# Performance work log

Measured on AMD Instinct MI355X. Metric: run time of the kernel, lower is better.

The kernel has to match this reference:

```python
import jax, jax.numpy as jnp
import numpy as np
import math

D_MODEL = 1024
LAYER_ID = 6
NUM_LAYERS = 12
B = 8
T = 2048


def setup_inputs() -> dict:
    key = jax.random.key(0)
    ks = jax.random.split(key, 5)
    r01 = LAYER_ID / (NUM_LAYERS - 1)
    r1a0 = 1.0 - LAYER_ID / NUM_LAYERS
    h = np.arange(D_MODEL, dtype=np.float32)
    w = (-5.0 + 8.0 * (h / (D_MODEL - 1)) ** (0.7 + 1.3 * r01)).astype(np.float32)
    zigzag = np.array([(i + 1) % 3 - 1 for i in range(D_MODEL)], np.float32) * 0.5
    u = (np.ones(D_MODEL, np.float32) * math.log(0.3) + zigzag).astype(np.float32)
    xinit = (h / D_MODEL).astype(np.float32)
    tmk = (xinit ** r1a0).reshape(1, 1, D_MODEL).astype(np.float32)
    tmv = (tmk + 0.3 * r01).astype(np.float32)
    tmr = (xinit ** (0.5 * r1a0)).reshape(1, 1, D_MODEL).astype(np.float32)
    s = 1.0 / math.sqrt(D_MODEL)
    Wk = jax.random.normal(ks[0], (D_MODEL, D_MODEL), jnp.float32) * s
    Wv = jax.random.normal(ks[1], (D_MODEL, D_MODEL), jnp.float32) * s
    Wr = jax.random.normal(ks[2], (D_MODEL, D_MODEL), jnp.float32) * s
    Wo = jax.random.normal(ks[3], (D_MODEL, D_MODEL), jnp.float32) * s
    x = jax.random.normal(ks[4], (B, T, D_MODEL), jnp.float32)
    return dict(
        x=x,
        w=jnp.asarray(w), u=jnp.asarray(u),
        time_mix_k=jnp.asarray(tmk), time_mix_v=jnpp if False else jnp.asarray(tmv), time_mix_r=jnp.asarray(tmr),
        Wk=Wk, Wv=Wv, Wr=Wr, Wo=Wo,
    )


def _wkv(w, u, k, v):
    # w,u: [C] (raw params); k,v: [B,T,C]. Numerically-stable RWKV scan.
    wn = -jnp.exp(w)  # decay (negative)

    def step(carry, kv):
        aa, bb, pp = carry  # each [B,C]
        kt, vt = kv         # [B,C]
        ww = u + kt
        p = jnp.maximum(pp, ww)
        e1 = jnp.exp(pp - p)
        e2 = jnp.exp(ww - p)
        y = (e1 * aa + e2 * vt) / (e1 * bb + e2)
        ww2 = pp + wn
        p2 = jnp.maximum(ww2, kt)
        e1b = jnp.exp(ww2 - p2)
        e2b = jnp.exp(kt - p2)
        return (e1b * aa + e2b * vt, e1b * bb + e2b, p2), y

    Bd, Td, Cd = k.shape
    init = (jnp.zeros((Bd, Cd), k.dtype), jnp.zeros((Bd, Cd), k.dtype),
            jnp.full((Bd, Cd), -1e38, k.dtype))
    kT = jnp.swapaxes(k, 0, 1)  # [T,B,C]
    vT = jnp.swapaxes(v, 0, 1)
    _, ys = jax.lax.scan(step, init, (kT, vT))
    return jnp.swapaxes(ys, 0, 1)  # [B,T,C]


def reference(x, w, u, time_mix_k, time_mix_v, time_mix_r, Wk, Wv, Wr, Wo):
    # token shift: zero-pad one step at the front of time, drop last
    xs = jnp.pad(x, ((0, 0), (1, 0), (0, 0)))[:, :-1]
    xk = x * time_mix_k + xs * (1.0 - time_mix_k)
    xv = x * time_mix_v + xs * (1.0 - time_mix_v)
    xr = x * time_mix_r + xs * (1.0 - time_mix_r)
    k = jnp.einsum('btc,dc->btd', xk, Wk)
    v = jnp.einsum('btc,dc->btd', xv, Wv)
    r = jnp.einsum('btc,dc->btd', xr, Wr)
    wkv = _wkv(w, u, k, v)
    rwkv = jax.nn.sigmoid(r) * wkv
    return jnp.einsum('btc,dc->btd', rwkv, Wo)
```

## Files before the change

kernel.cpp:

```cpp
#include <hip/hip_runtime.h>
#include <hip/hip_bf16.h>
#include <stdint.h>

#define DM     1024
#define BATCH  8
#define SEQ    2048
#define MROWS  (BATCH * SEQ)
#define NCH    16
#define CHL    (SEQ / NCH)

typedef unsigned short u16;
typedef __attribute__((ext_vector_type(8))) __bf16 bf16x8;
typedef __attribute__((ext_vector_type(4))) float  f32x4;

#define MB (1024ull * 1024ull)

__device__ __forceinline__ u16 f2bf(float f) {
    unsigned u = __float_as_uint(f);
    u += 0x7fffu + ((u >> 16) & 1u);
    return (u16)(u >> 16);
}
__device__ __forceinline__ float bf2f(u16 h) {
    return __uint_as_float(((unsigned)h) << 16);
}

__device__ __forceinline__ bool in_f32(const void* wraw) {
    return ((*(const unsigned*)wraw) & 0xFFFFu) == 0u;
}

__device__ __forceinline__ void ld16_lds(const u16* g, u16* l) {
    __builtin_amdgcn_global_load_lds(
        (const __attribute__((address_space(1))) void*)g,
        (__attribute__((address_space(3))) void*)l, 16, 0, 0);
}

__global__ __launch_bounds__(256) void mix_tile(
    const void* __restrict__ xraw,
    const void* __restrict__ tmkraw,
    const void* __restrict__ tmvraw,
    const void* __restrict__ tmrraw,
    const void* __restrict__ wraw,
    u16* __restrict__ xk, u16* __restrict__ xv, u16* __restrict__ xr)
{
    __shared__ u16 xt[18 * 1024];
    const bool f32i = in_f32(wraw);
    const int r0  = blockIdx.x * 16;
    const int t0  = r0 & (SEQ - 1);
    const int tid = threadIdx.x;
    const int c4  = tid * 4;

    float mk[4], mv[4], mr[4];
    if (f32i) {
        #pragma unroll
        for (int j = 0; j < 4; ++j) {
            mk[j] = ((const float*)tmkraw)[c4 + j];
            mv[j] = ((const float*)tmvraw)[c4 + j];
            mr[j] = ((const float*)tmrraw)[c4 + j];
        }
    } else {
        union { u16 h[4]; uint2 u; } a, b, c;
        a.u = *(const uint2*)((const u16*)tmkraw + c4);
        b.u = *(const uint2*)((const u16*)tmvraw + c4);
        c.u = *(const uint2*)((const u16*)tmrraw + c4);
        #pragma unroll
        for (int j = 0; j < 4; ++j) {
            mk[j] = bf2f(a.h[j]); mv[j] = bf2f(b.h[j]); mr[j] = bf2f(c.h[j]);
        }
    }

    #pragma unroll
    for (int p = 0; p < 9; ++p) {
        int lr = 2 * p + (tid >> 7);
        int gr = r0 - 1 + lr;
        if (lr == 0 && t0 == 0) gr = r0;
        if (gr >= MROWS) gr = r0;
        if (f32i) {
            const float* gp = (const float*)xraw + (size_t)gr * DM + (tid & 127) * 8;
            union { u16 h[8]; uint4 u; } t;
            #pragma unroll
            for (int j = 0; j < 8; ++j) t.h[j] = f2bf(gp[j]);
            *(uint4*)&xt[p * 2048 + tid * 8] = t.u;
        } else {
            const u16* gp = (const u16*)xraw + (size_t)gr * DM + (tid & 127) * 8;
            ld16_lds(gp, &xt[p * 2048 + (tid >> 6) * 512]);
        }
    }
    __syncthreads();

    const size_t obase = (size_t)r0 * DM + c4;
    #pragma unroll 4
    for (int rr = 0; rr < 16; ++rr) {
        union { u16 h[4]; uint2 u; } xa, xsv, ok, ov, orr;
        xa.u = *(const uint2*)&xt[(rr + 1) * 1024 + c4];
        float xf[4], sf[4];
        if (rr == 0 && t0 == 0) {
            #pragma unroll
            for (int j = 0; j < 4; ++j) sf[j] = 0.f;
        } else {
            xsv.u = *(const uint2*)&xt[rr * 1024 + c4];
            #pragma unroll
            for (int j = 0; j < 4; ++j) sf[j] = bf2f(xsv.h[j]);
        }
        #pragma unroll
        for (int j = 0; j < 4; ++j) xf[j] = bf2f(xa.h[j]);
        #pragma unroll
        for (int j = 0; j < 4; ++j) {
            float d = xf[j] - sf[j];
            ok.h[j]  = f2bf(sf[j] + mk[j] * d);
            ov.h[j]  = f2bf(sf[j] + mv[j] * d);
            orr.h[j] = f2bf(sf[j] + mr[j] * d);
        }
        size_t o = obase + (size_t)rr * DM;
        *(uint2*)(xk + o) = ok.u;
        *(uint2*)(xv + o) = ov.u;
        *(uint2*)(xr + o) = orr.u;
    }
}

__global__ void cast_w(const void* __restrict__ Wraw,
                       const void* __restrict__ wflag,
                       u16* __restrict__ Wb)
{
    int i = (blockIdx.x * 256 + threadIdx.x) << 2;
    if (in_f32(wflag)) {
        float4 wv = *(const float4*)((const float*)Wraw + i);
        union { u16 h[4]; uint2 u; } p;
        p.h[0] = f2bf(wv.x); p.h[1] = f2bf(wv.y);
        p.h[2] = f2bf(wv.z); p.h[3] = f2bf(wv.w);
        *(uint2*)(Wb + i) = p.u;
    } else {
        *(uint2*)(Wb + i) = *(const uint2*)((const u16*)Wraw + i);
    }
}

__device__ __forceinline__ void store_out(float* p, float v) { *p = v; }
__device__ __forceinline__ void store_out(u16*  p, float v) { *p = f2bf(v); }

template <typename OUT>
__global__ __launch_bounds__(256) void gemm_bt(const u16* __restrict__ A,
                                               const u16* __restrict__ B,
                                               OUT* __restrict__ C,
                                               int M, int N, int K)
{
    __shared__ u16 As[128 * 64];
    __shared__ u16 Bs[128 * 64];
    const int tid  = threadIdx.x;
    const int wave = tid >> 6, lane = tid & 63;
    const int wm   = wave >> 1, wn = wave & 1;
    const int lr   = lane & 15, quad = lane >> 4;
    const int tm   = blockIdx.y * 128, tn = blockIdx.x * 128;
    const int srow  = lane >> 3;
    const int skoff = (lane & 7) * 8;

    f32x4 acc[4][4] = {};

    for (int k0 = 0; k0 < K; k0 += 64) {
        #pragma unroll
        for (int i2 = 0; i2 < 4; ++i2) {
            int ch  = wave * 4 + i2;
            int row = ch * 8 + srow;
            ld16_lds(A + (size_t)(tm + row) * K + k0 + skoff, &As[ch * 512]);
            ld16_lds(B + (size_t)(tn + row) * K + k0 + skoff, &Bs[ch * 512]);
        }
        __syncthreads();
        #pragma unroll
        for (int kk2 = 0; kk2 < 2; ++kk2) {
            bf16x8 af[4], bfg[4];
            #pragma unroll
            for (int mi = 0; mi < 4; ++mi)
                af[mi] = *(const bf16x8*)&As[(wm * 64 + mi * 16 + lr) * 64 + kk2 * 32 + quad * 8];
            #pragma unroll
            for (int ni = 0; ni < 4; ++ni)
                bfg[ni] = *(const bf16x8*)&Bs[(wn * 64 + ni * 16 + lr) * 64 + kk2 * 32 + quad * 8];
            #pragma unroll
            for (int mi = 0; mi < 4; ++mi)
                #pragma unroll
                for (int ni = 0; ni < 4; ++ni)
                    acc[mi][ni] = __builtin_amdgcn_mfma_f32_16x16x32_bf16(
                        af[mi], bfg[ni], acc[mi][ni], 0, 0, 0);
        }
        __syncthreads();
    }
    #pragma unroll
    for (int mi = 0; mi < 4; ++mi)
        #pragma unroll
        for (int ni = 0; ni < 4; ++ni)
            #pragma unroll
            for (int r = 0; r < 4; ++r) {
                int row = tm + wm * 64 + mi * 16 + quad * 4 + r;
                int col = tn + wn * 64 + ni * 16 + lr;
                store_out(&C[(size_t)row * N + col], acc[mi][ni][r]);
            }
}

__device__ __forceinline__ float ldval(const float* p) { return *p; }
__device__ __forceinline__ float ldval(const u16*  p) { return bf2f(*p); }

template <typename KT>
__global__ __launch_bounds__(256) void wkv_phase1(
    const KT* __restrict__ kk, const u16* __restrict__ vv,
    const void* __restrict__ wraw,
    float* __restrict__ sa, float* __restrict__ sb, float* __restrict__ sp)
{
    const int gid = blockIdx.x * 256 + threadIdx.x;
    const int c   = gid & (DM - 1);
    const int ch  = (gid >> 10) & (NCH - 1);
    const int b   = gid >> 14;
    float wc = in_f32(wraw) ? ((const float*)wraw)[c] : bf2f(((const u16*)wraw)[c]);
    const float wn = -__expf(wc);

    const size_t base = ((size_t)b * SEQ + (size_t)ch * CHL) * DM + c;
    float la = 0.f, lb = 0.f, lp = -1e38f;

    float kb[8], vb[8];
    #pragma unroll
    for (int j = 0; j < 8; ++j) {
        size_t id = base + (size_t)j * DM;
        kb[j] = ldval(kk + id); vb[j] = ldval(vv + id);
    }
    for (int t0 = 0; t0 < CHL; t0 += 8) {
        const bool more = (t0 + 8) < CHL;
        float kn[8], vn[8];
        if (more) {
            size_t nb = base + (size_t)(t0 + 8) * DM;
            #pragma unroll
            for (int j = 0; j < 8; ++j) {
                size_t id = nb + (size_t)j * DM;
                kn[j] = ldval(kk + id); vn[j] = ldval(vv + id);
            }
        }
        #pragma unroll
        for (int j = 0; j < 8; ++j) {
            const float kt = kb[j], vt = vb[j];
            const float w2 = lp + wn;
            const float p2 = fmaxf(w2, kt);
            const float e1 = __expf(w2 - p2);
            const float e2 = __expf(kt - p2);
            la = e1 * la + e2 * vt;
            lb = e1 * lb + e2;
            lp = p2;
        }
        if (more) {
            #pragma unroll
            for (int j = 0; j < 8; ++j) { kb[j] = kn[j]; vb[j] = vn[j]; }
        }
    }
    const int sidx = ((b * NCH + ch) << 10) + c;
    sa[sidx] = la; sb[sidx] = lb; sp[sidx] = lp;
}

__global__ __launch_bounds__(256) void wkv_combine(
    float* __restrict__ sa, float* __restrict__ sb, float* __restrict__ sp,
    const void* __restrict__ wraw)
{
    const int gid = blockIdx.x * 256 + threadIdx.x;
    const int c   = gid & (DM - 1);
    const int b   = gid >> 10;
    float wc = in_f32(wraw) ? ((const float*)wraw)[c] : bf2f(((const u16*)wraw)[c]);
    const float lamL = -__expf(wc) * (float)CHL;

    float aa = 0.f, bb = 0.f, pp = -1e38f;
    #pragma unroll
    for (int j = 0; j < NCH; ++j) {
        const int idx = ((b * NCH + j) << 10) + c;
        const float la = sa[idx], lb = sb[idx], lp = sp[idx];
        sa[idx] = aa; sb[idx] = bb; sp[idx] = pp;
        const float w2 = pp + lamL;
        const float np = fmaxf(w2, lp);
        const float e1 = __expf(w2 - np);
        const float e2 = __expf(lp - np);
        aa = e1 * aa + e2 * la;
        bb = e1 * bb + e2 * lb;
        pp = np;
    }
}

template <typename KT>
__global__ __launch_bounds__(256) void wkv_phase3(
    const KT* __restrict__ kk, const u16* __restrict__ vv,
    const u16* __restrict__ rr,
    const float* __restrict__ sa, const float* __restrict__ sb,
    const float* __restrict__ sp,
    const void* __restrict__ wraw, const void* __restrict__ uraw,
    u16* __restrict__ out)
{
    const int gid = blockIdx.x * 256 + threadIdx.x;
    const int c   = gid & (DM - 1);
    const int ch  = (gid >> 10) & (NCH - 1);
    const int b   = gid >> 14;
    float wc, uc;
    if (in_f32(wraw)) {
        wc = ((const float*)wraw)[c]; uc = ((const float*)uraw)[c];
    } else {
        wc = bf2f(((const u16*)wraw)[c]); uc = bf2f(((const u16*)uraw)[c]);
    }
    const float wn = -__expf(wc);
    const float uu = uc;

    const int sidx = ((b * NCH + ch) << 10) + c;
    float aa = sa[sidx], bb = sb[sidx], pp = sp[sidx];

    const size_t base = ((size_t)b * SEQ + (size_t)ch * CHL) * DM + c;

    float kb[8], vb[8], rb[8];
    #pragma unroll
    for (int j = 0; j < 8; ++j) {
        size_t id = base + (size_t)j * DM;
        kb[j] = ldval(kk + id); vb[j] = ldval(vv + id); rb[j] = ldval(rr + id);
    }
    for (int t0 = 0; t0 < CHL; t0 += 8) {
        const bool more = (t0 + 8) < CHL;
        float kn[8], vn[8], rn[8];
        if (more) {
            size_t nb = base + (size_t)(t0 + 8) * DM;
            #pragma unroll
            for (int j = 0; j < 8; ++j) {
                size_t id = nb + (size_t)j * DM;
                kn[j] = ldval(kk + id); vn[j] = ldval(vv + id); rn[j] = ldval(rr + id);
            }
        }
        #pragma unroll
        for (int j = 0; j < 8; ++j) {
            const float kt = kb[j], vt = vb[j], rt = rb[j];
            const float ww = uu + kt;
            const float p  = fmaxf(pp, ww);
            const float e1 = __expf(pp - p);
            const float e2 = __expf(ww - p);
            const float y  = (e1 * aa + e2 * vt) / (e1 * bb + e2);
            const float w2 = pp + wn;
            const float p2 = fmaxf(w2, kt);
            const float e1b = __expf(w2 - p2);
            const float e2b = __expf(kt - p2);
            aa = e1b * aa + e2b * vt;
            bb = e1b * bb + e2b;
            pp = p2;
            const float sr = 1.f / (1.f + __expf(-rt));
            out[base + (size_t)(t0 + j) * DM] = f2bf(sr * y);
        }
        if (more) {
            #pragma unroll
            for (int j = 0; j < 8; ++j) { kb[j] = kn[j]; vb[j] = vn[j]; rb[j] = rn[j]; }
        }
    }
}

extern "C" void kernel_launch(void* const* d_in, const int* in_sizes, int n_in,
                              void* d_out, int out_size, void* d_ws, size_t ws_size,
                              hipStream_t stream)
{
    const void* x   = d_in[0];
    const void* w   = d_in[1];
    const void* u   = d_in[2];
    const void* tmk = d_in[3];
    const void* tmv = d_in[4];
    const void* tmr = d_in[5];
    const void* Wk  = d_in[6];
    const void* Wv  = d_in[7];
    const void* Wr  = d_in[8];
    const void* Wo  = d_in[9];

    char* base = (char*)d_ws;
    const bool kf32 = ws_size >= 168 * MB;
    u16* Wkb  = (u16*)(base);
    u16* Wvb  = (u16*)(base + 2 * MB);
    u16* Wrb  = (u16*)(base + 4 * MB);
    u16* Wob  = (u16*)(base + 6 * MB);
    u16* xk   = (u16*)(base + 8 * MB);
    u16* xv   = (u16*)(base + 40 * MB);
    u16* xr   = (u16*)(base + 72 * MB);
    void* kbuf = (void*)(base + 104 * MB);
    u16* vb   = xk;
    u16* rb   = xv;
    u16* rwkv = xr;
    float* sa = (float*)(base);
    float* sbuf = (float*)(base + 512 * 1024);
    float* sp = (float*)(base + 1024 * 1024);

    cast_w<<<DM * DM / 1024, 256, 0, stream>>>(Wk, w, Wkb);
    cast_w<<<DM * DM / 1024, 256, 0, stream>>>(Wv, w, Wvb);
    cast_w<<<DM * DM / 1024, 256, 0, stream>>>(Wr, w, Wrb);
    cast_w<<<DM * DM / 1024, 256, 0, stream>>>(Wo, w, Wob);
    mix_tile<<<MROWS / 16, 256, 0, stream>>>(x, tmk, tmv, tmr, w, xk, xv, xr);

    dim3 gg(DM / 128, MROWS / 128);
    if (kf32) {
        gemm_bt<float><<<gg, 256, 0, stream>>>(xk, Wkb, (float*)kbuf, MROWS, DM, DM);
    } else {
        gemm_bt<u16><<<gg, 256, 0, stream>>>(xk, Wkb, (u16*)kbuf, MROWS, DM, DM);
    }
    gemm_bt<u16><<<gg, 256, 0, stream>>>(xv, Wvb, vb, MROWS, DM, DM);
    gemm_bt<u16><<<gg, 256, 0, stream>>>(xr, Wrb, rb, MROWS, DM, DM);

    const int scan_threads = BATCH * NCH * DM;
    if (kf32) {
        wkv_phase1<float><<<scan_threads / 256, 256, 0, stream>>>(
            (const float*)kbuf, vb, w, sa, sbuf, sp);
        wkv_combine<<<BATCH * DM / 256, 256, 0, stream>>>(sa, sbuf, sp, w);
        wkv_phase3<float><<<scan_threads / 256, 256, 0, stream>>>(
            (const float*)kbuf, vb, rb, sa, sbuf, sp, w, u, rwkv);
    } else {
        wkv_phase1<u16><<<scan_threads / 256, 256, 0, stream>>>(
            (const u16*)kbuf, vb, w, sa, sbuf, sp);
        wkv_combine<<<BATCH * DM / 256, 256, 0, stream>>>(sa, sbuf, sp, w);
        wkv_phase3<u16><<<scan_threads / 256, 256, 0, stream>>>(
            (const u16*)kbuf, vb, rb, sa, sbuf, sp, w, u, rwkv);
    }

    gemm_bt<float><<<gg, 256, 0, stream>>>(rwkv, Wob, (float*)d_out, MROWS, DM, DM);
}
```

Baseline: 446.1 us.

## Batch K/V/R GEMMs into one launch with XCD-aware tile remap and padded LDS

Result: faster. 404.0 us (-9.4%).

```diff
diff --git a/kernel.cpp b/kernel.cpp
--- a/kernel.cpp
+++ b/kernel.cpp
@@ -8,6 +8,7 @@
 #define MROWS  (BATCH * SEQ)
 #define NCH    16
 #define CHL    (SEQ / NCH)
+#define CSTR   544
 
 typedef unsigned short u16;
 typedef __attribute__((ext_vector_type(8))) __bf16 bf16x8;
@@ -133,45 +134,61 @@
     }
 }
 
-__device__ __forceinline__ void store_out(float* p, float v) { *p = v; }
-__device__ __forceinline__ void store_out(u16*  p, float v) { *p = f2bf(v); }
-
-template <typename OUT>
-__global__ __launch_bounds__(256) void gemm_bt(const u16* __restrict__ A,
-                                               const u16* __restrict__ B,
-                                               OUT* __restrict__ C,
-                                               int M, int N, int K)
-{
-    __shared__ u16 As[128 * 64];
-    __shared__ u16 Bs[128 * 64];
+template <int NZ>
+__global__ __launch_bounds__(256) void gemm_bt(
+    const u16* __restrict__ A0, const u16* __restrict__ A1, const u16* __restrict__ A2,
+    const u16* __restrict__ B0, const u16* __restrict__ B1, const u16* __restrict__ B2,
+    void* __restrict__ C0, void* __restrict__ C1, void* __restrict__ C2,
+    int c0f32)
+{
+    __shared__ u16 As[16 * CSTR];
+    __shared__ u16 Bs[16 * CSTR];
+
+    const int lin = blockIdx.x + (blockIdx.y << 3) + (blockIdx.z << 10);
+    const int xcd = lin & 7;
+    const int idx = lin >> 3;
+    const int bxe = idx & 7;
+    const int t   = idx >> 3;
+    const int bye = xcd + ((t & 15) << 3);
+    const int z   = t >> 4;
+
+    const u16* A = (z == 0) ? A0 : (z == 1) ? A1 : A2;
+    const u16* B = (z == 0) ? B0 : (z == 1) ? B1 : B2;
+    void*      C = (z == 0) ? C0 : (z == 1) ? C1 : C2;
+    const bool f32out = (z == 0) && c0f32;
+
     const int tid  = threadIdx.x;
     const int wave = tid >> 6, lane = tid & 63;
     const int wm   = wave >> 1, wn = wave & 1;
     const int lr   = lane & 15, quad = lane >> 4;
-    const int tm   = blockIdx.y * 128, tn = blockIdx.x * 128;
+    const int tm   = bye * 128, tn = bxe * 128;
     const int srow  = lane >> 3;
     const int skoff = (lane & 7) * 8;
 
     f32x4 acc[4][4] = {};
 
-    for (int k0 = 0; k0 < K; k0 += 64) {
+    for (int k0 = 0; k0 < DM; k0 += 64) {
         #pragma unroll
         for (int i2 = 0; i2 < 4; ++i2) {
             int ch  = wave * 4 + i2;
             int row = ch * 8 + srow;
-            ld16_lds(A + (size_t)(tm + row) * K + k0 + skoff, &As[ch * 512]);
-            ld16_lds(B + (size_t)(tn + row) * K + k0 + skoff, &Bs[ch * 512]);
+            ld16_lds(A + (size_t)(tm + row) * DM + k0 + skoff, &As[ch * CSTR]);
+            ld16_lds(B + (size_t)(tn + row) * DM + k0 + skoff, &Bs[ch * CSTR]);
         }
         __syncthreads();
         #pragma unroll
         for (int kk2 = 0; kk2 < 2; ++kk2) {
             bf16x8 af[4], bfg[4];
             #pragma unroll
-            for (int mi = 0; mi < 4; ++mi)
-                af[mi] = *(const bf16x8*)&As[(wm * 64 + mi * 16 + lr) * 64 + kk2 * 32 + quad * 8];
-            #pragma unroll
-            for (int ni = 0; ni < 4; ++ni)
-                bfg[ni] = *(const bf16x8*)&Bs[(wn * 64 + ni * 16 + lr) * 64 + kk2 * 32 + quad * 8];
+            for (int mi = 0; mi < 4; ++mi) {
+                int r = wm * 64 + mi * 16 + lr;
+                af[mi] = *(const bf16x8*)&As[(r >> 3) * CSTR + (r & 7) * 64 + kk2 * 32 + quad * 8];
+            }
+            #pragma unroll
+            for (int ni = 0; ni < 4; ++ni) {
+                int r = wn * 64 + ni * 16 + lr;
+                bfg[ni] = *(const bf16x8*)&Bs[(r >> 3) * CSTR + (r & 7) * 64 + kk2 * 32 + quad * 8];
+            }
             #pragma unroll
             for (int mi = 0; mi < 4; ++mi)
                 #pragma unroll
@@ -189,7 +206,9 @@
             for (int r = 0; r < 4; ++r) {
                 int row = tm + wm * 64 + mi * 16 + quad * 4 + r;
                 int col = tn + wn * 64 + ni * 16 + lr;
-                store_out(&C[(size_t)row * N + col], acc[mi][ni][r]);
+                float v = acc[mi][ni][r];
+                if (f32out) ((float*)C)[(size_t)row * DM + col] = v;
+                else        ((u16*)C)[(size_t)row * DM + col]   = f2bf(v);
             }
 }
 
@@ -372,9 +391,9 @@
     u16* vb   = xk;
     u16* rb   = xv;
     u16* rwkv = xr;
-    float* sa = (float*)(base);
+    float* sa   = (float*)(base);
     float* sbuf = (float*)(base + 512 * 1024);
-    float* sp = (float*)(base + 1024 * 1024);
+    float* sp   = (float*)(base + 1024 * 1024);
 
     cast_w<<<DM * DM / 1024, 256, 0, stream>>>(Wk, w, Wkb);
     cast_w<<<DM * DM / 1024, 256, 0, stream>>>(Wv, w, Wvb);
@@ -382,14 +401,8 @@
     cast_w<<<DM * DM / 1024, 256, 0, stream>>>(Wo, w, Wob);
     mix_tile<<<MROWS / 16, 256, 0, stream>>>(x, tmk, tmv, tmr, w, xk, xv, xr);
 
-    dim3 gg(DM / 128, MROWS / 128);
-    if (kf32) {
-        gemm_bt<float><<<gg, 256, 0, stream>>>(xk, Wkb, (float*)kbuf, MROWS, DM, DM);
-    } else {
-        gemm_bt<u16><<<gg, 256, 0, stream>>>(xk, Wkb, (u16*)kbuf, MROWS, DM, DM);
-    }
-    gemm_bt<u16><<<gg, 256, 0, stream>>>(xv, Wvb, vb, MROWS, DM, DM);
-    gemm_bt<u16><<<gg, 256, 0, stream>>>(xr, Wrb, rb, MROWS, DM, DM);
+    gemm_bt<3><<<dim3(8, 128, 3), 256, 0, stream>>>(
+        xk, xv, xr, Wkb, Wvb, Wrb, kbuf, vb, rb, kf32 ? 1 : 0);
 
     const int scan_threads = BATCH * NCH * DM;
     if (kf32) {
@@ -406,5 +419,6 @@
             (const u16*)kbuf, vb, rb, sa, sbuf, sp, w, u, rwkv);
     }
 
-    gemm_bt<float><<<gg, 256, 0, stream>>>(rwkv, Wob, (float*)d_out, MROWS, DM, DM);
-}
+    gemm_bt<1><<<dim3(8, 128, 1), 256, 0, stream>>>(
+        rwkv, rwkv, rwkv, Wob, Wob, Wob, d_out, d_out, d_out, 1);
+}
```
